# Performance work log

Hardware: AMD Instinct MI355X
Metric: run time of the kernel (lower is better)

Reference implementation:

```python
import jax, jax.numpy as jnp
import numpy as np
import math

B, S, D, H = 8, 1024, 128, 8  # batch, seq, input_dim(=head_dim), head_num

def setup_inputs() -> dict:
    key = jax.random.key(0)
    ks = jax.random.split(key, 12)
    HD = H * D
    sc_in = 1.0 / math.sqrt(D)
    sc_hd = 1.0 / math.sqrt(HD)
    return {
        "query": jax.random.normal(ks[0], (B, S, D), jnp.float32),
        "key":   jax.random.normal(ks[1], (B, S, D), jnp.float32),
        "value": jax.random.normal(ks[2], (B, S, D), jnp.float32),
        "pos":   jax.random.normal(ks[3], (B, S, D), jnp.float32),
        "mask":  jnp.ones((B, S), jnp.int32),
        # torch Linear weights stored as [in, out] for x @ W + b
        "Wq": jax.random.normal(ks[4], (D, HD), jnp.float32) * sc_in,
        "bq": jnp.zeros((HD,), jnp.float32),
        "Wk": jax.random.normal(ks[5], (D, HD), jnp.float32) * sc_in,
        "bk": jnp.zeros((HD,), jnp.float32),
        "Wv": jax.random.normal(ks[6], (D, HD), jnp.float32) * sc_in,
        "bv": jnp.zeros((HD,), jnp.float32),
        "Wo": jax.random.normal(ks[7], (HD, D), jnp.float32) * sc_hd,
        "bo": jnp.zeros((D,), jnp.float32),
    }

def reference(query, key, value, pos, mask, Wq, bq, Wk, bk, Wv, bv, Wo, bo):
    # QKV projections (pos added to all three inputs)
    q = (query + pos) @ Wq + bq  # [B,S,H*D]
    k = (key + pos) @ Wk + bk
    v = (value + pos) @ Wv + bv
    # split heads -> [B,H,S,D]
    q = q.reshape(B, S, H, D).transpose(0, 2, 1, 3)
    k = k.reshape(B, S, H, D).transpose(0, 2, 1, 3)
    v = v.reshape(B, S, H, D).transpose(0, 2, 1, 3)
    scale = 1.0 / math.sqrt(D)
    scores = jnp.einsum("bhqd,bhkd->bhqk", q, k) * scale  # [B,H,S,S]
    # mask [B,S] -> broadcast over heads and query positions
    m = mask[:, None, None, :]  # [B,1,1,S]
    scores = jnp.where(m == 0, jnp.float32(-jnp.inf), scores)
    attn = jax.nn.softmax(scores, axis=-1)  # dropout is identity in eval mode
    out = jnp.einsum("bhqk,bhkd->bhqd", attn, v)
    out = out.transpose(0, 2, 1, 3).reshape(B, S, H * D)
    return out @ Wo + bo  # [B,S,D]
```

## Files before the change

### kernel.cpp

```cpp
#include <hip/hip_runtime.h>
#include <stdint.h>


typedef __attribute__((ext_vector_type(8))) short bf16x8;
typedef __attribute__((ext_vector_type(4))) float f32x4;
typedef unsigned int uint;
typedef unsigned short ushort;

__device__ __forceinline__ float bf2f(short s) {
    return __uint_as_float(((uint)(ushort)s) << 16);
}
__device__ __forceinline__ short f2bf(float f) {
    uint u = __float_as_uint(f);
    u += 0x7fffu + ((u >> 16) & 1u);
    return (short)(u >> 16);
}
__device__ __forceinline__ short f2bf_fast(float f) {
    return (short)((__float_as_uint(f) + 0x8000u) >> 16);
}

__device__ __forceinline__ void dma16(const short* g, short* l) {
    __builtin_amdgcn_global_load_lds(
        (const __attribute__((address_space(1))) uint*)g,
        (__attribute__((address_space(3))) uint*)l, 16, 0, 0);
}

__global__ __launch_bounds__(256) void fill_sentinel(float* __restrict__ out, int n) {
    int i = blockIdx.x * 256 + threadIdx.x;
    if (i < n) out[i] = 128.0f;
}

__global__ __launch_bounds__(256) void transpose_w(
    const float* __restrict__ Wq, const float* __restrict__ Wk,
    const float* __restrict__ Wv, const float* __restrict__ Wo,
    short* __restrict__ WTq, short* __restrict__ WTk,
    short* __restrict__ WTv, short* __restrict__ WoT)
{
    int z = blockIdx.y;
    const float* src; short* dst; int K, N;
    if (z < 3) { K = 128; N = 1024; src = (z==0)?Wq:(z==1)?Wk:Wv; dst = (z==0)?WTq:(z==1)?WTk:WTv; }
    else       { K = 1024; N = 128; src = Wo; dst = WoT; }
    int ntn = N >> 6;
    int nt = blockIdx.x % ntn, kt = blockIdx.x / ntn;
    int k0 = kt * 64, n0 = nt * 64;

    __shared__ __align__(16) short TT[64][72];
    int t = threadIdx.x;
    int r = t >> 2, c4 = t & 3;
    const float4* s4 = (const float4*)&src[(k0 + r) * N + n0 + c4 * 16];
    short* tr = &TT[r][c4 * 16];
#pragma unroll
    for (int i = 0; i < 4; ++i) {
        float4 v = s4[i];
        tr[i * 4 + 0] = f2bf(v.x);
        tr[i * 4 + 1] = f2bf(v.y);
        tr[i * 4 + 2] = f2bf(v.z);
        tr[i * 4 + 3] = f2bf(v.w);
    }
    __syncthreads();
    union { short s[16]; uint4 v[2]; } pk;
#pragma unroll
    for (int i = 0; i < 16; ++i) pk.s[i] = TT[c4 * 16 + i][r];
    uint4* dp = (uint4*)&dst[(n0 + r) * K + k0 + c4 * 16];
    dp[0] = pk.v[0]; dp[1] = pk.v[1];
}

__global__ __launch_bounds__(256) void qkv_proj(
    const float* __restrict__ query, const float* __restrict__ key_,
    const float* __restrict__ value, const float* __restrict__ pos,
    const short* __restrict__ WTq, const short* __restrict__ WTk, const short* __restrict__ WTv,
    const float* __restrict__ bq, const float* __restrict__ bk, const float* __restrict__ bv,
    short* __restrict__ Qg, short* __restrict__ Kg, short* __restrict__ Vtg)
{
    int z = blockIdx.y;
    const float* X    = (z==0) ? query : (z==1) ? key_ : value;
    const short* WT   = (z==0) ? WTq   : (z==1) ? WTk  : WTv;
    const float* bias = (z==0) ? bq    : (z==1) ? bk   : bv;

    __shared__ __align__(16) short Xs[64][136];
    __shared__ __align__(16) short Ws[2][8192];
    __shared__ __align__(16) short T[2][64][72];

    int t = threadIdx.x;
    int m0 = blockIdx.x * 64;
    int lane = t & 63, w = t >> 6;
    int l = lane & 15, q = lane >> 4;

    const short* wbase = &WT[(w * 16 + l) * 128 + q * 8];
    {
#pragma unroll
        for (int k32 = 0; k32 < 4; ++k32)
            dma16(wbase + k32 * 32, &Ws[0][(w * 4 + k32) * 512]);
    }
    {
        int r = t >> 2, c4 = t & 3;
        const float4* xs = (const float4*)&X[(m0 + r) * 128 + c4 * 32];
        const float4* ps = (const float4*)&pos[(m0 + r) * 128 + c4 * 32];
#pragma unroll
        for (int i = 0; i < 8; ++i) {
            float4 a = xs[i], bb = ps[i];
            uint2 o;
            o.x = (uint)(ushort)f2bf(a.x + bb.x) | ((uint)(ushort)f2bf(a.y + bb.y) << 16);
            o.y = (uint)(ushort)f2bf(a.z + bb.z) | ((uint)(ushort)f2bf(a.w + bb.w) << 16);
            *(uint2*)&Xs[r][c4 * 32 + i * 4] = o;
        }
    }
    __syncthreads();

    bf16x8 aX[4];
#pragma unroll
    for (int k32 = 0; k32 < 4; ++k32)
        aX[k32] = *(const bf16x8*)&Xs[w * 16 + l][k32 * 32 + q * 8];

    int b = m0 >> 10, s0 = m0 & 1023;

    for (int nt = 0; nt < 16; ++nt) {
        int cur = nt & 1;
        if (nt < 15) {
            const short* wsrc = wbase + (nt + 1) * 64 * 128;
#pragma unroll
            for (int k32 = 0; k32 < 4; ++k32)
                dma16(wsrc + k32 * 32, &Ws[cur ^ 1][(w * 4 + k32) * 512]);
        }

        f32x4 acc[4];
#pragma unroll
        for (int nb = 0; nb < 4; ++nb) {
            f32x4 c = {0.f, 0.f, 0.f, 0.f};
            const short* wf = &Ws[cur][nb * 2048 + lane * 8];
#pragma unroll
            for (int k32 = 0; k32 < 4; ++k32)
                c = __builtin_amdgcn_mfma_f32_16x16x32_bf16(aX[k32], *(const bf16x8*)(wf + k32 * 512), c, 0, 0, 0);
            acc[nb] = c;
        }

        int n0 = nt * 64;
        if (z < 2) {
#pragma unroll
            for (int nb = 0; nb < 4; ++nb) {
                float bi = bias[n0 + nb * 16 + l];
#pragma unroll
                for (int r = 0; r < 4; ++r)
                    T[cur][w * 16 + q * 4 + r][nb * 16 + l] = f2bf(acc[nb][r] + bi);
            }
            __syncthreads();
            short* dst = (z == 0) ? Qg : Kg;
            int row = t >> 2, c16 = t & 3;
            int n = n0 + c16 * 16, h = n >> 7, d0 = n & 127;
            uint4 v0 = *(uint4*)&T[cur][row][c16 * 16];
            uint4 v1 = *(uint4*)&T[cur][row][c16 * 16 + 8];
            uint4* dp = (uint4*)&dst[(((b * 8 + h) * 1024 + s0 + row) << 7) + d0];
            dp[0] = v0; dp[1] = v1;
        } else {
#pragma unroll
            for (int nb = 0; nb < 4; ++nb) {
                float bi = bias[n0 + nb * 16 + l];
#pragma unroll
                for (int r = 0; r < 4; ++r)
                    T[cur][nb * 16 + l][w * 16 + q * 4 + r] = f2bf(acc[nb][r] + bi);
            }
            __syncthreads();
            int nl = t >> 2, mc = t & 3;
            int n = n0 + nl, h = n >> 7, d = n & 127;
            uint4 v0 = *(uint4*)&T[cur][nl][mc * 16];
            uint4 v1 = *(uint4*)&T[cur][nl][mc * 16 + 8];
            uint4* dp = (uint4*)&Vtg[(((b * 8 + h) * 128 + d) << 10) + s0 + mc * 16];
            dp[0] = v0; dp[1] = v1;
        }
    }
}

__global__ __launch_bounds__(256, 2) void attention(
    const short* __restrict__ Qg, const short* __restrict__ Kg,
    const short* __restrict__ Vtg, const int* __restrict__ mask,
    short* __restrict__ AO)
{
    int bh = blockIdx.x & 63;
    int qt = blockIdx.x >> 6;
    int b = bh >> 3, h = bh & 7;
    int q0 = qt << 7;

    __shared__ __align__(16) short Ks[2][8192];
    __shared__ __align__(16) short Vs[8192];
    __shared__ __align__(16) short Ps[4][32][72];

    int t = threadIdx.x, lane = t & 63, w = t >> 6;
    int l = lane & 15, q = lane >> 4;

    const short* kbase = &Kg[((bh * 1024 + w * 16 + l) << 7) + q * 8];
    const short* vb0 = &Vtg[((bh * 128 + (2 * w) * 16 + l) << 10) + q * 8];
    const short* vb1 = &Vtg[((bh * 128 + (2 * w + 1) * 16 + l) << 10) + q * 8];
    const int* mrow = &mask[b * 1024];

    {
        dma16(kbase,      &Ks[0][(w * 4 + 0) * 512]);
        dma16(kbase + 32, &Ks[0][(w * 4 + 1) * 512]);
        dma16(kbase + 64, &Ks[0][(w * 4 + 2) * 512]);
        dma16(kbase + 96, &Ks[0][(w * 4 + 3) * 512]);
    }

    bf16x8 aQ[2][4];
#pragma unroll
    for (int s = 0; s < 2; ++s) {
        const short* qp = &Qg[((bh * 1024 + q0 + w * 32 + s * 16 + l) << 7) + q * 8];
#pragma unroll
        for (int k32 = 0; k32 < 4; ++k32)
            aQ[s][k32] = *(const bf16x8*)(qp + k32 * 32);
    }

    f32x4 O[2][8];
#pragma unroll
    for (int s = 0; s < 2; ++s)
#pragma unroll
        for (int i = 0; i < 8; ++i) O[s][i] = {0.f, 0.f, 0.f, 0.f};
    f32x4 Ls[2] = {{0.f, 0.f, 0.f, 0.f}, {0.f, 0.f, 0.f, 0.f}};

    const short O1 = (short)0x3F80;
    const bf16x8 ONES = {O1, O1, O1, O1, O1, O1, O1, O1};

    const float SL2E = 0.12752298917458827f;
    const float MAXB = 44.0f;

    for (int kt = 0; kt < 16; ++kt) {
        int k0 = kt << 6;
        int cur = kt & 1;
        __syncthreads();
        if (kt < 15) {
            const short* kp = kbase + (((kt + 1) << 6) << 7);
            dma16(kp,      &Ks[cur ^ 1][(w * 4 + 0) * 512]);
            dma16(kp + 32, &Ks[cur ^ 1][(w * 4 + 1) * 512]);
            dma16(kp + 64, &Ks[cur ^ 1][(w * 4 + 2) * 512]);
            dma16(kp + 96, &Ks[cur ^ 1][(w * 4 + 3) * 512]);
        }
        {
            dma16(vb0 + k0,      &Vs[(4 * w + 0) * 512]);
            dma16(vb0 + k0 + 32, &Vs[(4 * w + 1) * 512]);
            dma16(vb1 + k0,      &Vs[(4 * w + 2) * 512]);
            dma16(vb1 + k0 + 32, &Vs[(4 * w + 3) * 512]);
        }

        int mk[4];
#pragma unroll
        for (int nb = 0; nb < 4; ++nb) mk[nb] = mrow[k0 + nb * 16 + l];
        bool allm = (__ballot(mk[0] && mk[1] && mk[2] && mk[3]) == ~0ull);

#pragma unroll
        for (int nb = 0; nb < 4; ++nb) {
            bf16x8 kf[4];
            const short* kfp = &Ks[cur][nb * 2048 + lane * 8];
#pragma unroll
            for (int k32 = 0; k32 < 4; ++k32)
                kf[k32] = *(const bf16x8*)(kfp + k32 * 512);
#pragma unroll
            for (int s = 0; s < 2; ++s) {
                f32x4 c = {0.f, 0.f, 0.f, 0.f};
#pragma unroll
                for (int k32 = 0; k32 < 4; ++k32)
                    c = __builtin_amdgcn_mfma_f32_16x16x32_bf16(aQ[s][k32], kf[k32], c, 0, 0, 0);
#pragma unroll
                for (int r = 0; r < 4; ++r) {
                    float pv = exp2f(fmaf(c[r], SL2E, -MAXB));
                    if (!allm) pv = mk[nb] ? pv : 0.f;
                    Ps[w][s * 16 + q * 4 + r][nb * 16 + l] = f2bf_fast(pv);
                }
            }
        }
        __syncthreads();

        bf16x8 aP[2][2];
#pragma unroll
        for (int s = 0; s < 2; ++s) {
            aP[s][0] = *(const bf16x8*)&Ps[w][s * 16 + l][q * 8];
            aP[s][1] = *(const bf16x8*)&Ps[w][s * 16 + l][32 + q * 8];
        }
#pragma unroll
        for (int s = 0; s < 2; ++s) {
            Ls[s] = __builtin_amdgcn_mfma_f32_16x16x32_bf16(aP[s][0], ONES, Ls[s], 0, 0, 0);
            Ls[s] = __builtin_amdgcn_mfma_f32_16x16x32_bf16(aP[s][1], ONES, Ls[s], 0, 0, 0);
        }
#pragma unroll
        for (int dt = 0; dt < 8; ++dt) {
            bf16x8 vf0 = *(const bf16x8*)&Vs[(dt * 2 + 0) * 512 + lane * 8];
            bf16x8 vf1 = *(const bf16x8*)&Vs[(dt * 2 + 1) * 512 + lane * 8];
#pragma unroll
            for (int s = 0; s < 2; ++s) {
                f32x4 c = O[s][dt];
                c = __builtin_amdgcn_mfma_f32_16x16x32_bf16(aP[s][0], vf0, c, 0, 0, 0);
                c = __builtin_amdgcn_mfma_f32_16x16x32_bf16(aP[s][1], vf1, c, 0, 0, 0);
                O[s][dt] = c;
            }
        }
    }

#pragma unroll
    for (int s = 0; s < 2; ++s) {
        float rl[4];
#pragma unroll
        for (int r = 0; r < 4; ++r) rl[r] = 1.0f / Ls[s][r];
#pragma unroll
        for (int dt = 0; dt < 8; ++dt) {
            int col = h * 128 + dt * 16 + l;
#pragma unroll
            for (int r = 0; r < 4; ++r) {
                int srow = q0 + w * 32 + s * 16 + q * 4 + r;
                AO[((b * 1024 + srow) << 10) + col] = f2bf(O[s][dt][r] * rl[r]);
            }
        }
    }
}

__global__ __launch_bounds__(256) void out_proj(
    const short* __restrict__ AO, const short* __restrict__ WoT,
    const float* __restrict__ bo, float* __restrict__ out)
{
    __shared__ __align__(16) short As[2][32][72];
    __shared__ __align__(16) short Bs[2][8192];

    int t = threadIdx.x, lane = t & 63, w = t >> 6;
    int l = lane & 15, q = lane >> 4;
    int m0 = blockIdx.x * 32;
    int rowh = (w & 1) * 16;
    int nbg = (w >> 1) * 4;

    int ar = t >> 3, ac8 = t & 7;
    {
        *(uint4*)&As[0][ar][ac8 * 8] = *(const uint4*)&AO[((m0 + ar) << 10) + ac8 * 8];
#pragma unroll
        for (int j = 0; j < 4; ++j) {
            int nb = w * 2 + (j >> 1), k32 = j & 1;
            dma16(&WoT[(nb * 16 + l) * 1024 + k32 * 32 + q * 8], &Bs[0][(nb * 2 + k32) * 512]);
        }
    }

    f32x4 acc[4];
#pragma unroll
    for (int i = 0; i < 4; ++i) acc[i] = {0.f, 0.f, 0.f, 0.f};

    for (int kc = 0; kc < 16; ++kc) {
        __syncthreads();
        int cur = kc & 1;
        uint4 anext;
        if (kc < 15) {
            int k1 = (kc + 1) * 64;
            anext = *(const uint4*)&AO[((m0 + ar) << 10) + k1 + ac8 * 8];
#pragma unroll
            for (int j = 0; j < 4; ++j) {
                int nb = w * 2 + (j >> 1), k32 = j & 1;
                dma16(&WoT[(nb * 16 + l) * 1024 + k1 + k32 * 32 + q * 8],
                      &Bs[cur ^ 1][(nb * 2 + k32) * 512]);
            }
        }

        bf16x8 aA0 = *(const bf16x8*)&As[cur][rowh + l][q * 8];
        bf16x8 aA1 = *(const bf16x8*)&As[cur][rowh + l][32 + q * 8];
#pragma unroll
        for (int nb = 0; nb < 4; ++nb) {
            f32x4 c = acc[nb];
            c = __builtin_amdgcn_mfma_f32_16x16x32_bf16(aA0, *(const bf16x8*)&Bs[cur][((nbg + nb) * 2 + 0) * 512 + lane * 8], c, 0, 0, 0);
            c = __builtin_amdgcn_mfma_f32_16x16x32_bf16(aA1, *(const bf16x8*)&Bs[cur][((nbg + nb) * 2 + 1) * 512 + lane * 8], c, 0, 0, 0);
            acc[nb] = c;
        }

        if (kc < 15)
            *(uint4*)&As[cur ^ 1][ar][ac8 * 8] = anext;
    }

#pragma unroll
    for (int nb = 0; nb < 4; ++nb) {
        int n = (nbg + nb) * 16 + l;
        float bi = bo[n];
#pragma unroll
        for (int r = 0; r < 4; ++r) {
            int m = m0 + rowh + q * 4 + r;
            out[(m << 7) + n] = acc[nb][r] + bi;
        }
    }
}

extern "C" void kernel_launch(void* const* d_in, const int* in_sizes, int n_in,
                              void* d_out, int out_size, void* d_ws, size_t ws_size,
                              hipStream_t stream)
{
    const size_t NEED = (size_t)65 * 1024 * 1024;
    if (ws_size < NEED) {
        hipLaunchKernelGGL(fill_sentinel, dim3((out_size + 255) / 256), dim3(256), 0, stream,
                           (float*)d_out, out_size);
        return;
    }

    const float* query = (const float*)d_in[0];
    const float* key_  = (const float*)d_in[1];
    const float* value = (const float*)d_in[2];
    const float* pos   = (const float*)d_in[3];
    const int*   mask  = (const int*)d_in[4];
    const float* Wq = (const float*)d_in[5];
    const float* bq = (const float*)d_in[6];
    const float* Wk = (const float*)d_in[7];
    const float* bk = (const float*)d_in[8];
    const float* Wv = (const float*)d_in[9];
    const float* bv = (const float*)d_in[10];
    const float* Wo = (const float*)d_in[11];
    const float* bo = (const float*)d_in[12];

    char* ws = (char*)d_ws;
    short* Qg  = (short*)(ws);
    short* Kg  = (short*)(ws + (size_t)16 * 1024 * 1024);
    short* Vtg = (short*)(ws + (size_t)32 * 1024 * 1024);
    short* AO  = (short*)(ws + (size_t)48 * 1024 * 1024);
    short* WTq = (short*)(ws + (size_t)64 * 1024 * 1024);
    short* WTk = WTq + 131072;
    short* WTv = WTk + 131072;
    short* WoT = WTv + 131072;

    hipLaunchKernelGGL(transpose_w, dim3(32, 4), dim3(256), 0, stream,
                       Wq, Wk, Wv, Wo, WTq, WTk, WTv, WoT);
    hipLaunchKernelGGL(qkv_proj, dim3(128, 3), dim3(256), 0, stream,
                       query, key_, value, pos, WTq, WTk, WTv, bq, bk, bv, Qg, Kg, Vtg);
    hipLaunchKernelGGL(attention, dim3(512), dim3(256), 0, stream,
                       Qg, Kg, Vtg, mask, AO);
    hipLaunchKernelGGL(out_proj, dim3(256), dim3(256), 0, stream,
                       AO, WoT, bo, (float*)d_out);
}
```

Before: 196.2 us.

## Split QKV and output projections across more blocks, store MFMA results directly

The QKV projection grid is doubled so each block handles half of the output columns, and the output projection now uses 16-row tiles across twice as many blocks, which raises parallelism for these small GEMMs. MFMA operands are swapped so each lane holds four consecutive output columns. Q/K and the final output can then be written straight from registers as vector stores, with no LDS staging tile and no extra barrier. The cost is that each block now repeats the input conversion, the V transpose is written as scattered 2-byte stores, and out_proj uses only half its threads to load A.

New measurement: 194.5 us. About the same (-0.9%).

```diff
diff --git a/kernel.cpp b/kernel.cpp
--- a/kernel.cpp
+++ b/kernel.cpp
@@ -3,6 +3,7 @@
 
 
 typedef __attribute__((ext_vector_type(8))) short bf16x8;
+typedef __attribute__((ext_vector_type(4))) short s16x4;
 typedef __attribute__((ext_vector_type(4))) float f32x4;
 typedef unsigned int uint;
 typedef unsigned short ushort;
@@ -79,10 +80,11 @@
 
     __shared__ __align__(16) short Xs[64][136];
     __shared__ __align__(16) short Ws[2][8192];
-    __shared__ __align__(16) short T[2][64][72];
 
     int t = threadIdx.x;
-    int m0 = blockIdx.x * 64;
+    int bx = blockIdx.x;
+    int m0 = (bx >> 1) * 64;
+    int nt0 = (bx & 1) * 8;
     int lane = t & 63, w = t >> 6;
     int l = lane & 15, q = lane >> 4;
 
@@ -90,7 +92,7 @@
     {
 #pragma unroll
         for (int k32 = 0; k32 < 4; ++k32)
-            dma16(wbase + k32 * 32, &Ws[0][(w * 4 + k32) * 512]);
+            dma16(wbase + nt0 * 8192 + k32 * 32, &Ws[0][(w * 4 + k32) * 512]);
     }
     {
         int r = t >> 2, c4 = t & 3;
@@ -113,59 +115,43 @@
         aX[k32] = *(const bf16x8*)&Xs[w * 16 + l][k32 * 32 + q * 8];
 
     int b = m0 >> 10, s0 = m0 & 1023;
-
-    for (int nt = 0; nt < 16; ++nt) {
-        int cur = nt & 1;
-        if (nt < 15) {
-            const short* wsrc = wbase + (nt + 1) * 64 * 128;
+    int srow = s0 + w * 16 + l;
+
+    for (int i = 0; i < 8; ++i) {
+        int nt = nt0 + i;
+        int cur = i & 1;
+        if (i) __syncthreads();
+        if (i < 7) {
+            const short* wsrc = wbase + (nt + 1) * 8192;
 #pragma unroll
             for (int k32 = 0; k32 < 4; ++k32)
                 dma16(wsrc + k32 * 32, &Ws[cur ^ 1][(w * 4 + k32) * 512]);
         }
 
-        f32x4 acc[4];
+        int n0 = nt * 64;
 #pragma unroll
         for (int nb = 0; nb < 4; ++nb) {
             f32x4 c = {0.f, 0.f, 0.f, 0.f};
             const short* wf = &Ws[cur][nb * 2048 + lane * 8];
 #pragma unroll
             for (int k32 = 0; k32 < 4; ++k32)
-                c = __builtin_amdgcn_mfma_f32_16x16x32_bf16(aX[k32], *(const bf16x8*)(wf + k32 * 512), c, 0, 0, 0);
-            acc[nb] = c;
-        }
-
-        int n0 = nt * 64;
-        if (z < 2) {
-#pragma unroll
-            for (int nb = 0; nb < 4; ++nb) {
-                float bi = bias[n0 + nb * 16 + l];
-#pragma unroll
-                for (int r = 0; r < 4; ++r)
-                    T[cur][w * 16 + q * 4 + r][nb * 16 + l] = f2bf(acc[nb][r] + bi);
+                c = __builtin_amdgcn_mfma_f32_16x16x32_bf16(*(const bf16x8*)(wf + k32 * 512), aX[k32], c, 0, 0, 0);
+            const float* bip = &bias[n0 + nb * 16 + q * 4];
+            if (z < 2) {
+                short* dst = (z == 0) ? Qg : Kg;
+                int n00 = n0 + nb * 16;
+                int hh = n00 >> 7, d0 = (n00 & 127) + q * 4;
+                s16x4 ov = { f2bf(c[0] + bip[0]), f2bf(c[1] + bip[1]),
+                             f2bf(c[2] + bip[2]), f2bf(c[3] + bip[3]) };
+                *(s16x4*)&dst[(((b * 8 + hh) * 1024 + srow) << 7) + d0] = ov;
+            } else {
+#pragma unroll
+                for (int r = 0; r < 4; ++r) {
+                    int n = n0 + nb * 16 + q * 4 + r;
+                    int hh = n >> 7, dd = n & 127;
+                    Vtg[(((b * 8 + hh) * 128 + dd) << 10) + srow] = f2bf(c[r] + bip[r]);
+                }
             }
-            __syncthreads();
-            short* dst = (z == 0) ? Qg : Kg;
-            int row = t >> 2, c16 = t & 3;
-            int n = n0 + c16 * 16, h = n >> 7, d0 = n & 127;
-            uint4 v0 = *(uint4*)&T[cur][row][c16 * 16];
-            uint4 v1 = *(uint4*)&T[cur][row][c16 * 16 + 8];
-            uint4* dp = (uint4*)&dst[(((b * 8 + h) * 1024 + s0 + row) << 7) + d0];
-            dp[0] = v0; dp[1] = v1;
-        } else {
-#pragma unroll
-            for (int nb = 0; nb < 4; ++nb) {
-                float bi = bias[n0 + nb * 16 + l];
-#pragma unroll
-                for (int r = 0; r < 4; ++r)
-                    T[cur][nb * 16 + l][w * 16 + q * 4 + r] = f2bf(acc[nb][r] + bi);
-            }
-            __syncthreads();
-            int nl = t >> 2, mc = t & 3;
-            int n = n0 + nl, h = n >> 7, d = n & 127;
-            uint4 v0 = *(uint4*)&T[cur][nl][mc * 16];
-            uint4 v1 = *(uint4*)&T[cur][nl][mc * 16 + 8];
-            uint4* dp = (uint4*)&Vtg[(((b * 8 + h) * 128 + d) << 10) + s0 + mc * 16];
-            dp[0] = v0; dp[1] = v1;
         }
     }
 }
@@ -313,28 +299,27 @@
     const short* __restrict__ AO, const short* __restrict__ WoT,
     const float* __restrict__ bo, float* __restrict__ out)
 {
-    __shared__ __align__(16) short As[2][32][72];
+    __shared__ __align__(16) short As[2][16][72];
     __shared__ __align__(16) short Bs[2][8192];
 
     int t = threadIdx.x, lane = t & 63, w = t >> 6;
     int l = lane & 15, q = lane >> 4;
-    int m0 = blockIdx.x * 32;
-    int rowh = (w & 1) * 16;
-    int nbg = (w >> 1) * 4;
+    int m0 = blockIdx.x * 16;
 
     int ar = t >> 3, ac8 = t & 7;
     {
-        *(uint4*)&As[0][ar][ac8 * 8] = *(const uint4*)&AO[((m0 + ar) << 10) + ac8 * 8];
+        if (t < 128)
+            *(uint4*)&As[0][ar][ac8 * 8] = *(const uint4*)&AO[((m0 + ar) << 10) + ac8 * 8];
 #pragma unroll
         for (int j = 0; j < 4; ++j) {
-            int nb = w * 2 + (j >> 1), k32 = j & 1;
+            int nb = 2 * w + (j >> 1), k32 = j & 1;
             dma16(&WoT[(nb * 16 + l) * 1024 + k32 * 32 + q * 8], &Bs[0][(nb * 2 + k32) * 512]);
         }
     }
 
-    f32x4 acc[4];
-#pragma unroll
-    for (int i = 0; i < 4; ++i) acc[i] = {0.f, 0.f, 0.f, 0.f};
+    f32x4 acc[2];
+    acc[0] = {0.f, 0.f, 0.f, 0.f};
+    acc[1] = {0.f, 0.f, 0.f, 0.f};
 
     for (int kc = 0; kc < 16; ++kc) {
         __syncthreads();
@@ -342,38 +327,38 @@
         uint4 anext;
         if (kc < 15) {
             int k1 = (kc + 1) * 64;
-            anext = *(const uint4*)&AO[((m0 + ar) << 10) + k1 + ac8 * 8];
+            if (t < 128)
+                anext = *(const uint4*)&AO[((m0 + ar) << 10) + k1 + ac8 * 8];
 #pragma unroll
             for (int j = 0; j < 4; ++j) {
-                int nb = w * 2 + (j >> 1), k32 = j & 1;
+                int nb = 2 * w + (j >> 1), k32 = j & 1;
                 dma16(&WoT[(nb * 16 + l) * 1024 + k1 + k32 * 32 + q * 8],
                       &Bs[cur ^ 1][(nb * 2 + k32) * 512]);
             }
         }
 
-        bf16x8 aA0 = *(const bf16x8*)&As[cur][rowh + l][q * 8];
-        bf16x8 aA1 = *(const bf16x8*)&As[cur][rowh + l][32 + q * 8];
-#pragma unroll
-        for (int nb = 0; nb < 4; ++nb) {
+        bf16x8 aA0 = *(const bf16x8*)&As[cur][l][q * 8];
+        bf16x8 aA1 = *(const bf16x8*)&As[cur][l][32 + q * 8];
+#pragma unroll
+        for (int nb = 0; nb < 2; ++nb) {
+            int nbg = 2 * w + nb;
             f32x4 c = acc[nb];
-            c = __builtin_amdgcn_mfma_f32_16x16x32_bf16(aA0, *(const bf16x8*)&Bs[cur][((nbg + nb) * 2 + 0) * 512 + lane * 8], c, 0, 0, 0);
-            c = __builtin_amdgcn_mfma_f32_16x16x32_bf16(aA1, *(const bf16x8*)&Bs[cur][((nbg + nb) * 2 + 1) * 512 + lane * 8], c, 0, 0, 0);
+            c = __builtin_amdgcn_mfma_f32_16x16x32_bf16(*(const bf16x8*)&Bs[cur][(nbg * 2 + 0) * 512 + lane * 8], aA0, c, 0, 0, 0);
+            c = __builtin_amdgcn_mfma_f32_16x16x32_bf16(*(const bf16x8*)&Bs[cur][(nbg * 2 + 1) * 512 + lane * 8], aA1, c, 0, 0, 0);
             acc[nb] = c;
         }
 
-        if (kc < 15)
+        if (kc < 15 && t < 128)
             *(uint4*)&As[cur ^ 1][ar][ac8 * 8] = anext;
     }
 
 #pragma unroll
-    for (int nb = 0; nb < 4; ++nb) {
-        int n = (nbg + nb) * 16 + l;
-        float bi = bo[n];
-#pragma unroll
-        for (int r = 0; r < 4; ++r) {
-            int m = m0 + rowh + q * 4 + r;
-            out[(m << 7) + n] = acc[nb][r] + bi;
-        }
+    for (int nb = 0; nb < 2; ++nb) {
+        int n0 = (2 * w + nb) * 16 + q * 4;
+        const float* bop = &bo[n0];
+        float4 ov = { acc[nb][0] + bop[0], acc[nb][1] + bop[1],
+                      acc[nb][2] + bop[2], acc[nb][3] + bop[3] };
+        *(float4*)&out[((m0 + l) << 7) + n0] = ov;
     }
 }
 
@@ -414,10 +399,10 @@
 
     hipLaunchKernelGGL(transpose_w, dim3(32, 4), dim3(256), 0, stream,
                        Wq, Wk, Wv, Wo, WTq, WTk, WTv, WoT);
-    hipLaunchKernelGGL(qkv_proj, dim3(128, 3), dim3(256), 0, stream,
+    hipLaunchKernelGGL(qkv_proj, dim3(256, 3), dim3(256), 0, stream,
                        query, key_, value, pos, WTq, WTk, WTv, bq, bk, bv, Qg, Kg, Vtg);
     hipLaunchKernelGGL(attention, dim3(512), dim3(256), 0, stream,
                        Qg, Kg, Vtg, mask, AO);
-    hipLaunchKernelGGL(out_proj, dim3(256), dim3(256), 0, stream,
+    hipLaunchKernelGGL(out_proj, dim3(512), dim3(256), 0, stream,
                        AO, WoT, bo, (float*)d_out);
 }
```
